# Performance work log

Hardware: AMD Instinct MI355X
Metric: run time of the kernel (lower is better)

Reference implementation:

```python
import jax, jax.numpy as jnp
import numpy as np

HIDDEN = 2048
HEADS = 32
HEAD_DIM = HIDDEN // HEADS  # 64
MAX_POS = 512
TABLE = 2 * MAX_POS - 1  # 1023


def setup_inputs() -> dict:
    key = jax.random.key(0)
    k = jax.random.split(key, 6)
    B, S = 16, 512
    return {
        "hidden_states": jax.random.normal(k[0], (B, S, HIDDEN), dtype=jnp.float32),
        "wq": jax.random.normal(k[1], (HIDDEN, HIDDEN), dtype=jnp.float32) * 0.02,
        "wk": jax.random.normal(k[2], (HIDDEN, HIDDEN), dtype=jnp.float32) * 0.02,
        "wv": jax.random.normal(k[3], (HIDDEN, HIDDEN), dtype=jnp.float32) * 0.02,
        "wo": jax.random.normal(k[4], (HIDDEN, HIDDEN), dtype=jnp.float32) * 0.02,
        "rel_pos": jax.random.normal(k[5], (TABLE, HEAD_DIM), dtype=jnp.float32),
    }


def _rel_bias(rel_pos, seq_len):
    pos = jnp.arange(seq_len)
    rel = pos[None, :] - pos[:, None] + (MAX_POS - 1)  # [S, S]
    rel = jnp.clip(rel, 0, TABLE - 1)
    return rel_pos[rel].mean(axis=-1)  # [S, S]


def reference(hidden_states, wq, wk, wv, wo, rel_pos):
    B, S, _ = hidden_states.shape
    scale = jnp.sqrt(jnp.float32(HEAD_DIM))
    # nn.Linear(x) = x @ W.T
    q = (hidden_states @ wq.T).reshape(B, S, HEADS, HEAD_DIM).transpose(0, 2, 1, 3)
    k = (hidden_states @ wk.T).reshape(B, S, HEADS, HEAD_DIM).transpose(0, 2, 1, 3)
    v = (hidden_states @ wv.T).reshape(B, S, HEADS, HEAD_DIM).transpose(0, 2, 1, 3)
    scores = jnp.einsum("bhqd,bhkd->bhqk", q, k) / scale
    scores = scores + _rel_bias(rel_pos, S)[None, None]  # seq_len <= 512 path
    attn = jax.nn.softmax(scores, axis=-1)
    ctx = jnp.einsum("bhqk,bhkd->bhqd", attn, v)
    ctx = ctx.transpose(0, 2, 1, 3).reshape(B, S, HIDDEN)
    return ctx @ wo.T
```

## Files before the change

kernel.cpp:

```cpp
#include <hip/hip_runtime.h>

typedef __attribute__((ext_vector_type(8))) short bf16x8;
typedef __attribute__((ext_vector_type(4))) float f32x4;
typedef const __attribute__((address_space(3))) unsigned short* lds_cp;

#define DEVI __device__ __forceinline__

template <int N> struct IC { static constexpr int v = N; };

DEVI unsigned short f2bf(float f) {
  union { float f; unsigned u; } v; v.f = f;
  unsigned r = v.u + 0x7FFFu + ((v.u >> 16) & 1u);
  return (unsigned short)(r >> 16);
}

DEVI void gload16(const void* g, void* l) {
  __builtin_amdgcn_global_load_lds(
      (const __attribute__((address_space(1))) unsigned int*)g,
      (__attribute__((address_space(3))) unsigned int*)l, 16, 0, 0);
}

template <int OFF>
DEVI bf16x8 lreadT(lds_cp p) {
  bf16x8 r;
  asm volatile("ds_read_b128 %0, %1 offset:%2" : "=v"(r) : "v"(p), "i"(OFF));
  return r;
}

#define MFMA16(a, b, c) __builtin_amdgcn_mfma_f32_16x16x32_bf16(a, b, c, 0, 0, 0)

__global__ void cvt_kernel(const float* __restrict__ in,
                           unsigned short* __restrict__ out, int n4) {
  int i = blockIdx.x * blockDim.x + threadIdx.x;
  if (i < n4) {
    float4 v = ((const float4*)in)[i];
    ushort4 o;
    o.x = f2bf(v.x); o.y = f2bf(v.y); o.z = f2bf(v.z); o.w = f2bf(v.w);
    ((ushort4*)out)[i] = o;
  }
}

__global__ void cvt4_kernel(const float* __restrict__ a,
                            const float* __restrict__ b,
                            const float* __restrict__ c,
                            const float* __restrict__ d,
                            unsigned short* __restrict__ out) {
  int i = blockIdx.x * blockDim.x + threadIdx.x;
  const int w = i >> 20, l = i & 1048575;
  const float* s = (w == 0) ? a : (w == 1) ? b : (w == 2) ? c : d;
  float4 v = ((const float4*)s)[l];
  ushort4 o;
  o.x = f2bf(v.x); o.y = f2bf(v.y); o.z = f2bf(v.z); o.w = f2bf(v.w);
  ((ushort4*)out)[i] = o;
}

__global__ void bias_kernel(const float* __restrict__ rel_pos,
                            float* __restrict__ bias1d) {
  int t = blockIdx.x * blockDim.x + threadIdx.x;
  if (t < 1023) {
    const float* r = rel_pos + t * 64;
    float s = 0.f;
#pragma unroll
    for (int d = 0; d < 64; ++d) s += r[d];
    bias1d[t] = s * (1.44269504f / 64.0f);
  }
}

template <int MODE, int NT>
__global__ __launch_bounds__(512, 2) void gemm256(
    const unsigned short* __restrict__ A, const unsigned short* __restrict__ B,
    void* __restrict__ Cout, void* __restrict__ Cout2, void* __restrict__ Cout3) {
  __shared__ unsigned short As[2][16384];
  __shared__ unsigned short Bs[2][16384];

  const int tid = threadIdx.x;
  const int logical = (blockIdx.x & 7) * (4 * NT) + (blockIdx.x >> 3);
  const int nt = logical % NT, mt = logical / NT;
  const int m0 = mt * 256, n0 = nt * 256;
  const int lane = tid & 63, wid = tid >> 6;
  const int wr = wid >> 2, wc = wid & 3;
  const int g = lane >> 4, c = lane & 15;

  const unsigned short* Ag = A + (size_t)m0 * 2048u;
  const unsigned short* Bg = B + (size_t)n0 * 2048u;

  const int srow = tid >> 3, sj = (tid & 7) ^ (srow & 7);
  const unsigned short* pA0[2];
  const unsigned short* pA1[2];
  const unsigned short* pB0[2];
  const unsigned short* pB1[2];
  unsigned short* lA0[2];
  unsigned short* lA1[2];
  unsigned short* lB0[2];
  unsigned short* lB1[2];
#pragma unroll
  for (int ch = 0; ch < 2; ++ch) {
    const int row = ch * 64 + srow;
    pA0[ch] = Ag + (size_t)row * 2048u + sj * 8;
    pA1[ch] = Ag + (size_t)(128 + row) * 2048u + sj * 8;
    pB0[ch] = Bg + (size_t)row * 2048u + sj * 8;
    pB1[ch] = Bg + (size_t)(128 + row) * 2048u + sj * 8;
    const int slot = ch * 512 + tid;
    lA0[ch] = &As[0][slot * 8];
    lA1[ch] = &As[0][8192 + slot * 8];
    lB0[ch] = &Bs[0][slot * 8];
    lB1[ch] = &Bs[0][8192 + slot * 8];
  }

  lds_cp aA[4][2], aB[2][2];
#pragma unroll
  for (int mi = 0; mi < 4; ++mi) {
    const int r = wr * 128 + mi * 16 + c;
#pragma unroll
    for (int kk = 0; kk < 2; ++kk)
      aA[mi][kk] = (lds_cp)&As[0][r * 64 + (((kk * 4 + g) ^ (r & 7)) * 8)];
  }
#pragma unroll
  for (int ni = 0; ni < 2; ++ni) {
    const int r = wc * 64 + ni * 16 + c;
#pragma unroll
    for (int kk = 0; kk < 2; ++kk)
      aB[ni][kk] = (lds_cp)&Bs[0][r * 64 + (((kk * 4 + g) ^ (r & 7)) * 8)];
  }

  f32x4 acc[8][4];
#pragma unroll
  for (int i = 0; i < 8; ++i)
#pragma unroll
    for (int j = 0; j < 4; ++j) acc[i][j] = (f32x4){0.f, 0.f, 0.f, 0.f};

  bf16x8 af[4][2], bq0[2][2], bq1[2][2];

#pragma unroll
  for (int ch = 0; ch < 2; ++ch) {
    gload16(pA0[ch], lA0[ch]);
    gload16(pA1[ch], lA1[ch]);
    gload16(pB0[ch], lB0[ch]);
    gload16(pB1[ch], lB1[ch]);
  }
#pragma unroll
  for (int ch = 0; ch < 2; ++ch) {
    gload16(pA0[ch] + 64, lA0[ch] + 16384);
    gload16(pA1[ch] + 64, lA1[ch] + 16384);
    gload16(pB0[ch] + 64, lB0[ch] + 16384);
    gload16(pB1[ch] + 64, lB1[ch] + 16384);
  }
  asm volatile("s_waitcnt vmcnt(8)" ::: "memory");
  __builtin_amdgcn_sched_barrier(0);
  __builtin_amdgcn_s_barrier();

  auto ktile = [&](auto B_, auto S_, auto LD_, int kt) {
    constexpr int BOFF = decltype(B_)::v;
    constexpr int S = decltype(S_)::v;
    constexpr int LD = decltype(LD_)::v;

#pragma unroll
    for (int mi = 0; mi < 4; ++mi)
#pragma unroll
      for (int kk = 0; kk < 2; ++kk) af[mi][kk] = lreadT<BOFF>(aA[mi][kk]);
#pragma unroll
    for (int ni = 0; ni < 2; ++ni)
#pragma unroll
      for (int kk = 0; kk < 2; ++kk) bq0[ni][kk] = lreadT<BOFF>(aB[ni][kk]);
    asm volatile("s_waitcnt lgkmcnt(8)");
    __builtin_amdgcn_s_barrier();
    asm volatile("s_waitcnt lgkmcnt(0)");
    __builtin_amdgcn_sched_barrier(0);
    __builtin_amdgcn_s_setprio(1);
#pragma unroll
    for (int kk = 0; kk < 2; ++kk)
#pragma unroll
      for (int mi = 0; mi < 4; ++mi)
#pragma unroll
        for (int ni = 0; ni < 2; ++ni)
          acc[mi][ni] = MFMA16(af[mi][kk], bq0[ni][kk], acc[mi][ni]);
    __builtin_amdgcn_s_setprio(0);
    __builtin_amdgcn_s_barrier();

#pragma unroll
    for (int ni = 0; ni < 2; ++ni)
#pragma unroll
      for (int kk = 0; kk < 2; ++kk)
        bq1[ni][kk] = lreadT<BOFF + 4096>(aB[ni][kk]);
    __builtin_amdgcn_s_barrier();
    asm volatile("s_waitcnt lgkmcnt(0)");
    __builtin_amdgcn_sched_barrier(0);
    __builtin_amdgcn_s_setprio(1);
#pragma unroll
    for (int kk = 0; kk < 2; ++kk)
#pragma unroll
      for (int mi = 0; mi < 4; ++mi)
#pragma unroll
        for (int ni = 0; ni < 2; ++ni)
          acc[mi][ni + 2] = MFMA16(af[mi][kk], bq1[ni][kk], acc[mi][ni + 2]);
    __builtin_amdgcn_s_setprio(0);
    __builtin_amdgcn_s_barrier();

#pragma unroll
    for (int mi = 0; mi < 4; ++mi)
#pragma unroll
      for (int kk = 0; kk < 2; ++kk)
        af[mi][kk] = lreadT<BOFF + 8192>(aA[mi][kk]);
    if (kt + 2 < 32) {
      gload16(pB0[0] + S, lB0[0] + LD);
      gload16(pB0[1] + S, lB0[1] + LD);
      gload16(pB1[0] + S, lB1[0] + LD);
      gload16(pB1[1] + S, lB1[1] + LD);
    }
    __builtin_amdgcn_s_barrier();
    asm volatile("s_waitcnt lgkmcnt(0)");
    __builtin_amdgcn_sched_barrier(0);
    __builtin_amdgcn_s_setprio(1);
#pragma unroll
    for (int kk = 0; kk < 2; ++kk)
#pragma unroll
      for (int mi = 0; mi < 4; ++mi)
#pragma unroll
        for (int ni = 0; ni < 2; ++ni)
          acc[mi + 4][ni] = MFMA16(af[mi][kk], bq0[ni][kk], acc[mi + 4][ni]);
    __builtin_amdgcn_s_setprio(0);
    __builtin_amdgcn_s_barrier();

    if (kt + 2 < 32) {
      gload16(pA0[0] + S, lA0[0] + LD);
      gload16(pA0[1] + S, lA0[1] + LD);
      gload16(pA1[0] + S, lA1[0] + LD);
      gload16(pA1[1] + S, lA1[1] + LD);
    }
    if (kt < 30) {
      asm volatile("s_waitcnt vmcnt(8)" ::: "memory");
    } else {
      asm volatile("s_waitcnt vmcnt(0)" ::: "memory");
    }
    __builtin_amdgcn_sched_barrier(0);
    __builtin_amdgcn_s_barrier();
    __builtin_amdgcn_s_setprio(1);
#pragma unroll
    for (int kk = 0; kk < 2; ++kk)
#pragma unroll
      for (int mi = 0; mi < 4; ++mi)
#pragma unroll
        for (int ni = 0; ni < 2; ++ni)
          acc[mi + 4][ni + 2] = MFMA16(af[mi][kk], bq1[ni][kk], acc[mi + 4][ni + 2]);
    __builtin_amdgcn_s_setprio(0);
    __builtin_amdgcn_s_barrier();
  };

  for (int t2 = 0; t2 < 16; ++t2) {
    ktile(IC<0>{}, IC<128>{}, IC<0>{}, 2 * t2);
    ktile(IC<32768>{}, IC<192>{}, IC<16384>{}, 2 * t2 + 1);
#pragma unroll
    for (int ch = 0; ch < 2; ++ch) {
      pA0[ch] += 128; pA1[ch] += 128; pB0[ch] += 128; pB1[ch] += 128;
    }
  }

  const int rbase = m0 + wr * 128 + g * 4;
  const int cbase = n0 + wc * 64 + c;
  if (MODE == 0) {
    float* O = (float*)Cout;
#pragma unroll
    for (int mi = 0; mi < 8; ++mi)
#pragma unroll
      for (int ni = 0; ni < 4; ++ni)
#pragma unroll
        for (int rr = 0; rr < 4; ++rr)
          O[(size_t)(rbase + mi * 16 + rr) * 2048u + (cbase + ni * 16)] =
              acc[mi][ni][rr];
  } else {
    const int qsel = cbase >> 11;
    if (qsel < 2) {
      unsigned short* O = (unsigned short*)(qsel == 0 ? Cout : Cout2);
#pragma unroll
      for (int mi = 0; mi < 8; ++mi)
#pragma unroll
        for (int ni = 0; ni < 4; ++ni)
#pragma unroll
          for (int rr = 0; rr < 4; ++rr)
            O[(size_t)(rbase + mi * 16 + rr) * 2048u +
              ((cbase + ni * 16) & 2047)] = f2bf(acc[mi][ni][rr]);
    } else {
      unsigned short* O = (unsigned short*)Cout3;
#pragma unroll
      for (int mi = 0; mi < 8; ++mi)
#pragma unroll
        for (int ni = 0; ni < 4; ++ni) {
          const int row = rbase + mi * 16;
          const int col = (cbase + ni * 16) & 2047;
          const int bq_ = row >> 9, s = row & 511;
          const int hh = col >> 6, dd = col & 63;
          ushort4 o;
          o.x = f2bf(acc[mi][ni][0]);
          o.y = f2bf(acc[mi][ni][1]);
          o.z = f2bf(acc[mi][ni][2]);
          o.w = f2bf(acc[mi][ni][3]);
          *(ushort4*)(O + ((size_t)((bq_ * 32 + hh) * 64 + dd) << 9) + s) = o;
        }
    }
  }
}

__global__ __launch_bounds__(256, 3) void attn_kernel(
    const unsigned short* __restrict__ Q, const unsigned short* __restrict__ K,
    const unsigned short* __restrict__ VT, const float* __restrict__ bias1d,
    unsigned short* __restrict__ CTX) {
  __shared__ unsigned short Ksh[2][4096];
  __shared__ unsigned short Vsh[2][4096];
  __shared__ unsigned short Pb[4][2048];
  __shared__ float bl[1024];

  const int tid = threadIdx.x;
  const int wave = tid >> 6;
  const int lane = tid & 63;
  const int g = lane >> 4, c = lane & 15;

  const int logical = (blockIdx.x & 7) * 256 + (blockIdx.x >> 3);
  const int qc = logical & 3;
  const int bh = logical >> 2;
  const int b = bh >> 5, h = bh & 31;
  const int qrow0 = qc * 128 + wave * 32;

  for (int i = tid; i < 1023; i += 256) bl[i] = bias1d[i];

  bf16x8 aq[2][2];
  {
    const unsigned short* qb =
        Q + (size_t)(b * 512 + qrow0 + c) * 2048u + h * 64 + g * 8;
#pragma unroll
    for (int mi = 0; mi < 2; ++mi)
#pragma unroll
      for (int kk = 0; kk < 2; ++kk)
        aq[mi][kk] = *(const bf16x8*)(qb + mi * 16 * 2048 + kk * 32);
  }

  const unsigned short* kgb = K + (size_t)(b * 512) * 2048u + h * 64;
  const unsigned short* vgb = VT + (size_t)(bh * 64) * 512u;

  auto stage = [&](int buf, int kt) {
#pragma unroll
    for (int half = 0; half < 2; ++half) {
      const int slot = half * 256 + wave * 64 + lane;
      const int row = slot >> 3;
      const int j = (slot & 7) ^ (row & 7);
      gload16(kgb + (size_t)(kt * 64 + row) * 2048u + j * 8,
              &Ksh[buf][slot * 8]);
      gload16(vgb + (size_t)row * 512u + kt * 64 + j * 8, &Vsh[buf][slot * 8]);
    }
  };

  f32x4 o[2][4];
#pragma unroll
  for (int mi = 0; mi < 2; ++mi)
#pragma unroll
    for (int di = 0; di < 4; ++di) o[mi][di] = (f32x4){0.f, 0.f, 0.f, 0.f};
  float lreg[2][4];
#pragma unroll
  for (int mi = 0; mi < 2; ++mi)
#pragma unroll
    for (int rr = 0; rr < 4; ++rr) lreg[mi][rr] = 0.f;

  stage(0, 0);
  __syncthreads();

  const float SSCALE = 0.125f * 1.44269504f;

  for (int kt = 0; kt < 8; ++kt) {
    const int buf = kt & 1;
    if (kt < 7) stage(buf ^ 1, kt + 1);

    f32x4 s[2][4];
#pragma unroll
    for (int ni = 0; ni < 4; ++ni) {
      const unsigned short* kr = &Ksh[buf][(ni * 16 + c) * 64];
      bf16x8 bk0 = *(const bf16x8*)(kr + ((0 + g) ^ (c & 7)) * 8);
      bf16x8 bk1 = *(const bf16x8*)(kr + ((4 + g) ^ (c & 7)) * 8);
#pragma unroll
      for (int mi = 0; mi < 2; ++mi) {
        f32x4 z = (f32x4){0.f, 0.f, 0.f, 0.f};
        z = MFMA16(aq[mi][0], bk0, z);
        z = MFMA16(aq[mi][1], bk1, z);
        s[mi][ni] = z;
      }
    }

    unsigned short* pw = &Pb[wave][0];
#pragma unroll
    for (int mi = 0; mi < 2; ++mi)
#pragma unroll
      for (int rr = 0; rr < 4; ++rr) {
        const int prow = mi * 16 + g * 4 + rr;
        const int off0 = kt * 64 + c - (qrow0 + prow) + 511;
        float e0 = __builtin_amdgcn_exp2f(s[mi][0][rr] * SSCALE + bl[off0]);
        float e1 = __builtin_amdgcn_exp2f(s[mi][1][rr] * SSCALE + bl[off0 + 16]);
        float e2 = __builtin_amdgcn_exp2f(s[mi][2][rr] * SSCALE + bl[off0 + 32]);
        float e3 = __builtin_amdgcn_exp2f(s[mi][3][rr] * SSCALE + bl[off0 + 48]);
        lreg[mi][rr] += (e0 + e1) + (e2 + e3);
        const int rx = prow * 64, sw = (c >> 3) ^ (prow & 7), cl = c & 7;
        pw[rx + ((0 ^ sw) * 8 | cl)] = f2bf(e0);
        pw[rx + ((2 ^ sw) * 8 | cl)] = f2bf(e1);
        pw[rx + ((4 ^ sw) * 8 | cl)] = f2bf(e2);
        pw[rx + ((6 ^ sw) * 8 | cl)] = f2bf(e3);
      }

#pragma unroll
    for (int kk = 0; kk < 2; ++kk) {
      bf16x8 pa0 =
          *(const bf16x8*)(pw + (0 + c) * 64 + ((kk * 4 + g) ^ (c & 7)) * 8);
      bf16x8 pa1 =
          *(const bf16x8*)(pw + (16 + c) * 64 + ((kk * 4 + g) ^ (c & 7)) * 8);
#pragma unroll
      for (int di = 0; di < 4; ++di) {
        bf16x8 vb = *(const bf16x8*)(&Vsh[buf][(di * 16 + c) * 64 +
                                               ((kk * 4 + g) ^ (c & 7)) * 8]);
        o[0][di] = MFMA16(pa0, vb, o[0][di]);
        o[1][di] = MFMA16(pa1, vb, o[1][di]);
      }
    }
    __syncthreads();
  }

#pragma unroll
  for (int mi = 0; mi < 2; ++mi)
#pragma unroll
    for (int rr = 0; rr < 4; ++rr) {
      float l = lreg[mi][rr];
      l += __shfl_xor(l, 1);
      l += __shfl_xor(l, 2);
      l += __shfl_xor(l, 4);
      l += __shfl_xor(l, 8);
      const float rl = __builtin_amdgcn_rcpf(l);
      unsigned short* ob =
          CTX + (size_t)(b * 512 + qrow0 + mi * 16 + g * 4 + rr) * 2048u +
          h * 64 + c;
#pragma unroll
      for (int di = 0; di < 4; ++di) ob[di * 16] = f2bf(o[mi][di][rr] * rl);
    }
}

extern "C" void kernel_launch(void* const* d_in, const int* in_sizes, int n_in,
                              void* d_out, int out_size, void* d_ws,
                              size_t ws_size, hipStream_t stream) {
  const float* x = (const float*)d_in[0];
  const float* wq = (const float*)d_in[1];
  const float* wk = (const float*)d_in[2];
  const float* wv = (const float*)d_in[3];
  const float* wo = (const float*)d_in[4];
  const float* rel = (const float*)d_in[5];

  char* ws = (char*)d_ws;
  unsigned short* xb = (unsigned short*)(ws);
  unsigned short* wqb = (unsigned short*)(ws + 33554432);
  unsigned short* wob = wqb + 3 * 4194304;
  unsigned short* qb = (unsigned short*)(ws + 67108864);
  unsigned short* kb = qb + 16777216;
  unsigned short* vt = kb + 16777216;
  float* bias1 = (float*)(ws + 167772160);
  unsigned short* ctx = xb;

  cvt_kernel<<<16384, 256, 0, stream>>>(x, xb, 4194304);
  cvt4_kernel<<<16384, 256, 0, stream>>>(wq, wk, wv, wo, wqb);
  bias_kernel<<<4, 256, 0, stream>>>(rel, bias1);

  gemm256<3, 24><<<768, 512, 0, stream>>>(xb, wqb, qb, kb, vt);

  attn_kernel<<<2048, 256, 0, stream>>>(qb, kb, vt, bias1, ctx);

  gemm256<0, 8><<<256, 512, 0, stream>>>(ctx, wob, (float*)d_out, nullptr,
                                         nullptr);
}
```

Baseline: 343.1 us.

## Software-pipeline LDS fragment reads and cut barriers in GEMM k-loop

Restructures the GEMM inner k-tile loop so the next tile's A/B low fragments are prefetched from LDS before the final MFMA block. All A fragments (low and high halves) are now held in separate register sets, and staged lgkmcnt waits let MFMAs start while the remaining LDS reads complete. Per-tile workgroup barriers drop from roughly eight to two, and both global prefetch batches are issued together. This aims to hide LDS latency and barrier stalls, at the cost of more live vector registers, which may reduce occupancy.

Result: slower. 461.1 us (+34.4%).

```diff
diff --git a/kernel.cpp b/kernel.cpp
--- a/kernel.cpp
+++ b/kernel.cpp
@@ -28,6 +28,8 @@
 }
 
 #define MFMA16(a, b, c) __builtin_amdgcn_mfma_f32_16x16x32_bf16(a, b, c, 0, 0, 0)
+#define LGKM(n) asm volatile("s_waitcnt lgkmcnt(" #n ")")
+#define SBAR() __builtin_amdgcn_sched_barrier(0)
 
 __global__ void cvt_kernel(const float* __restrict__ in,
                            unsigned short* __restrict__ out, int n4) {
@@ -129,7 +131,7 @@
 #pragma unroll
     for (int j = 0; j < 4; ++j) acc[i][j] = (f32x4){0.f, 0.f, 0.f, 0.f};
 
-  bf16x8 af[4][2], bq0[2][2], bq1[2][2];
+  bf16x8 afl[4][2], afh[4][2], bq0[2][2], bq1[2][2];
 
 #pragma unroll
   for (int ch = 0; ch < 2; ++ch) {
@@ -146,94 +148,99 @@
     gload16(pB1[ch] + 64, lB1[ch] + 16384);
   }
   asm volatile("s_waitcnt vmcnt(8)" ::: "memory");
-  __builtin_amdgcn_sched_barrier(0);
+  SBAR();
   __builtin_amdgcn_s_barrier();
-
-  auto ktile = [&](auto B_, auto S_, auto LD_, int kt) {
+#pragma unroll
+  for (int mi = 0; mi < 4; ++mi)
+#pragma unroll
+    for (int kk = 0; kk < 2; ++kk) afl[mi][kk] = lreadT<0>(aA[mi][kk]);
+#pragma unroll
+  for (int ni = 0; ni < 2; ++ni)
+#pragma unroll
+    for (int kk = 0; kk < 2; ++kk) bq0[ni][kk] = lreadT<0>(aB[ni][kk]);
+
+  auto ktile = [&](auto B_, auto NB_, auto S_, auto LD_, int kt) {
     constexpr int BOFF = decltype(B_)::v;
+    constexpr int NBOFF = decltype(NB_)::v;
     constexpr int S = decltype(S_)::v;
     constexpr int LD = decltype(LD_)::v;
 
 #pragma unroll
-    for (int mi = 0; mi < 4; ++mi)
-#pragma unroll
-      for (int kk = 0; kk < 2; ++kk) af[mi][kk] = lreadT<BOFF>(aA[mi][kk]);
-#pragma unroll
-    for (int ni = 0; ni < 2; ++ni)
-#pragma unroll
-      for (int kk = 0; kk < 2; ++kk) bq0[ni][kk] = lreadT<BOFF>(aB[ni][kk]);
-    asm volatile("s_waitcnt lgkmcnt(8)");
-    __builtin_amdgcn_s_barrier();
-    asm volatile("s_waitcnt lgkmcnt(0)");
-    __builtin_amdgcn_sched_barrier(0);
-    __builtin_amdgcn_s_setprio(1);
-#pragma unroll
-    for (int kk = 0; kk < 2; ++kk)
-#pragma unroll
-      for (int mi = 0; mi < 4; ++mi)
-#pragma unroll
-        for (int ni = 0; ni < 2; ++ni)
-          acc[mi][ni] = MFMA16(af[mi][kk], bq0[ni][kk], acc[mi][ni]);
-    __builtin_amdgcn_s_setprio(0);
-    __builtin_amdgcn_s_barrier();
-
-#pragma unroll
     for (int ni = 0; ni < 2; ++ni)
 #pragma unroll
       for (int kk = 0; kk < 2; ++kk)
         bq1[ni][kk] = lreadT<BOFF + 4096>(aB[ni][kk]);
+#pragma unroll
+    for (int mi = 0; mi < 4; ++mi)
+#pragma unroll
+      for (int kk = 0; kk < 2; ++kk)
+        afh[mi][kk] = lreadT<BOFF + 8192>(aA[mi][kk]);
+
+    LGKM(12);
+    SBAR();
+    __builtin_amdgcn_s_setprio(1);
+#pragma unroll
+    for (int kk = 0; kk < 2; ++kk)
+#pragma unroll
+      for (int mi = 0; mi < 4; ++mi)
+#pragma unroll
+        for (int ni = 0; ni < 2; ++ni)
+          acc[mi][ni] = MFMA16(afl[mi][kk], bq0[ni][kk], acc[mi][ni]);
+    __builtin_amdgcn_s_setprio(0);
+
+    LGKM(8);
+    SBAR();
+    __builtin_amdgcn_s_setprio(1);
+#pragma unroll
+    for (int kk = 0; kk < 2; ++kk)
+#pragma unroll
+      for (int mi = 0; mi < 4; ++mi)
+#pragma unroll
+        for (int ni = 0; ni < 2; ++ni)
+          acc[mi][ni + 2] = MFMA16(afl[mi][kk], bq1[ni][kk], acc[mi][ni + 2]);
+    __builtin_amdgcn_s_setprio(0);
+
+    LGKM(0);
+    SBAR();
     __builtin_amdgcn_s_barrier();
-    asm volatile("s_waitcnt lgkmcnt(0)");
-    __builtin_amdgcn_sched_barrier(0);
-    __builtin_amdgcn_s_setprio(1);
-#pragma unroll
-    for (int kk = 0; kk < 2; ++kk)
-#pragma unroll
-      for (int mi = 0; mi < 4; ++mi)
-#pragma unroll
-        for (int ni = 0; ni < 2; ++ni)
-          acc[mi][ni + 2] = MFMA16(af[mi][kk], bq1[ni][kk], acc[mi][ni + 2]);
-    __builtin_amdgcn_s_setprio(0);
-    __builtin_amdgcn_s_barrier();
-
-#pragma unroll
-    for (int mi = 0; mi < 4; ++mi)
-#pragma unroll
-      for (int kk = 0; kk < 2; ++kk)
-        af[mi][kk] = lreadT<BOFF + 8192>(aA[mi][kk]);
     if (kt + 2 < 32) {
       gload16(pB0[0] + S, lB0[0] + LD);
       gload16(pB0[1] + S, lB0[1] + LD);
       gload16(pB1[0] + S, lB1[0] + LD);
       gload16(pB1[1] + S, lB1[1] + LD);
-    }
-    __builtin_amdgcn_s_barrier();
-    asm volatile("s_waitcnt lgkmcnt(0)");
-    __builtin_amdgcn_sched_barrier(0);
-    __builtin_amdgcn_s_setprio(1);
-#pragma unroll
-    for (int kk = 0; kk < 2; ++kk)
-#pragma unroll
-      for (int mi = 0; mi < 4; ++mi)
-#pragma unroll
-        for (int ni = 0; ni < 2; ++ni)
-          acc[mi + 4][ni] = MFMA16(af[mi][kk], bq0[ni][kk], acc[mi + 4][ni]);
-    __builtin_amdgcn_s_setprio(0);
-    __builtin_amdgcn_s_barrier();
-
-    if (kt + 2 < 32) {
       gload16(pA0[0] + S, lA0[0] + LD);
       gload16(pA0[1] + S, lA0[1] + LD);
       gload16(pA1[0] + S, lA1[0] + LD);
       gload16(pA1[1] + S, lA1[1] + LD);
     }
+
+    __builtin_amdgcn_s_setprio(1);
+#pragma unroll
+    for (int kk = 0; kk < 2; ++kk)
+#pragma unroll
+      for (int mi = 0; mi < 4; ++mi)
+#pragma unroll
+        for (int ni = 0; ni < 2; ++ni)
+          acc[mi + 4][ni] = MFMA16(afh[mi][kk], bq0[ni][kk], acc[mi + 4][ni]);
+    __builtin_amdgcn_s_setprio(0);
+
     if (kt < 30) {
       asm volatile("s_waitcnt vmcnt(8)" ::: "memory");
     } else {
       asm volatile("s_waitcnt vmcnt(0)" ::: "memory");
     }
-    __builtin_amdgcn_sched_barrier(0);
+    SBAR();
     __builtin_amdgcn_s_barrier();
+    if (kt + 1 < 32) {
+#pragma unroll
+      for (int mi = 0; mi < 4; ++mi)
+#pragma unroll
+        for (int kk = 0; kk < 2; ++kk) afl[mi][kk] = lreadT<NBOFF>(aA[mi][kk]);
+#pragma unroll
+      for (int ni = 0; ni < 2; ++ni)
+#pragma unroll
+        for (int kk = 0; kk < 2; ++kk) bq0[ni][kk] = lreadT<NBOFF>(aB[ni][kk]);
+    }
     __builtin_amdgcn_s_setprio(1);
 #pragma unroll
     for (int kk = 0; kk < 2; ++kk)
@@ -241,14 +248,13 @@
       for (int mi = 0; mi < 4; ++mi)
 #pragma unroll
         for (int ni = 0; ni < 2; ++ni)
-          acc[mi + 4][ni + 2] = MFMA16(af[mi][kk], bq1[ni][kk], acc[mi + 4][ni + 2]);
+          acc[mi + 4][ni + 2] = MFMA16(afh[mi][kk], bq1[ni][kk], acc[mi + 4][ni + 2]);
     __builtin_amdgcn_s_setprio(0);
-    __builtin_amdgcn_s_barrier();
   };
 
   for (int t2 = 0; t2 < 16; ++t2) {
-    ktile(IC<0>{}, IC<128>{}, IC<0>{}, 2 * t2);
-    ktile(IC<32768>{}, IC<192>{}, IC<16384>{}, 2 * t2 + 1);
+    ktile(IC<0>{}, IC<32768>{}, IC<128>{}, IC<0>{}, 2 * t2);
+    ktile(IC<32768>{}, IC<0>{}, IC<192>{}, IC<16384>{}, 2 * t2 + 1);
 #pragma unroll
     for (int ch = 0; ch < 2; ++ch) {
       pA0[ch] += 128; pA1[ch] += 128; pB0[ch] += 128; pB1[ch] += 128;
```
